# Kernel tuning notes

Measured on AMD Instinct MI355X. Metric: run time of the kernel, lower is better.

The kernel has to match this reference:

```python
import jax, jax.numpy as jnp
import numpy as np

S, B, E = 4096, 8, 1024
H, D, K = 16, 64, 64  # num_heads, head_dim, proj_dim
TAU = 1.0

def setup_inputs() -> dict:
    key = jax.random.key(0)
    ks = jax.random.split(key, 6)
    return {
        "encoder_output": jax.random.normal(ks[0], (S, B, E), dtype=jnp.float32),
        "Wk": jax.random.normal(ks[1], (E, E), dtype=jnp.float32) * (E ** -0.5),
        "bk": jax.random.normal(ks[2], (E,), dtype=jnp.float32) * 0.02,
        "Wv": jax.random.normal(ks[3], (E, E), dtype=jnp.float32) * (E ** -0.5),
        "bv": jax.random.normal(ks[4], (E,), dtype=jnp.float32) * 0.02,
        "random_matrices": jax.random.normal(ks[5], (H, K, D), dtype=jnp.float32),
        "mask": jnp.zeros((S, B, 1, 1), dtype=bool),
    }

def reference(encoder_output, Wk, bk, Wv, bv, random_matrices, mask):
    # k/v projections: [S,B,E] -> [S,B,H,D]
    k = (encoder_output @ Wk.T + bk).reshape(S, B, H, D)
    v = (encoder_output @ Wv.T + bv).reshape(S, B, H, D)
    # build_random_matrices (reparam_proj=False): divide by tau
    rm = random_matrices / TAU
    # rrf random feature map: scale by head_dim**-0.5 / tau, project, sin/cos concat
    x = k * (D ** -0.5) / TAU
    proj = jnp.einsum('sbhd,hkd->sbhk', x, rm)  # [S,B,H,K]
    phi_k = jnp.concatenate([jnp.sin(proj), jnp.cos(proj)], axis=-1) * (K ** -0.5)  # [S,B,H,2K]
    phi_k = jnp.where(mask, 0.0, phi_k)
    # s/z linear-attention state accumulation over seq_len
    s = jnp.einsum('sbhk,sbhd->bhkd', phi_k, v)  # [B,H,2K,D]
    z = jnp.sum(phi_k, axis=0)                   # [B,H,2K]
    return (s, z, rm)
```

## Files before the change

kernel.cpp:

```cpp
#include <hip/hip_runtime.h>
#include <hip/hip_bf16.h>
#include <stdint.h>


typedef short bf16x8 __attribute__((ext_vector_type(8)));
typedef float f32x4 __attribute__((ext_vector_type(4)));

__device__ __forceinline__ unsigned short f2bf(float f) {
  unsigned u = __float_as_uint(f);
  u += 0x7fffu + ((u >> 16) & 1u);
  return (unsigned short)(u >> 16);
}
__device__ __forceinline__ unsigned pack2(float a, float b) {
  return (unsigned)f2bf(a) | ((unsigned)f2bf(b) << 16);
}

#define OFF_WC   0ull
#define OFF_BC   4194304ull
#define OFF_AB   4202496ull
#define OFF_PS   272637952ull
#define OFF_PZ   306192384ull

__global__ __launch_bounds__(256) void k_conv_enc(const float* __restrict__ enc,
                                                  unsigned short* __restrict__ ab) {
  size_t i = ((size_t)blockIdx.x * 256 + threadIdx.x) * 8;
  const float4* p = (const float4*)(enc + i);
  float4 a = p[0], b = p[1];
  uint4 o;
  o.x = pack2(a.x, a.y); o.y = pack2(a.z, a.w);
  o.z = pack2(b.x, b.y); o.w = pack2(b.z, b.w);
  *(uint4*)(ab + i) = o;
}

__global__ __launch_bounds__(256) void k_prep_w(const float* __restrict__ Wk,
                                                const float* __restrict__ bk,
                                                const float* __restrict__ Wv,
                                                const float* __restrict__ bv,
                                                const float* __restrict__ rm,
                                                unsigned short* __restrict__ Wc,
                                                float* __restrict__ bc) {
  __shared__ float rv[64];
  int f = blockIdx.x;
  int tid = threadIdx.x;
  int e0 = tid * 4;
  if (f < 1024) {
    int h = f >> 6, kk = f & 63;
    if (tid < 64) rv[tid] = rm[(size_t)((h << 6) + kk) * 64 + tid] * 0.125f;
    __syncthreads();
    float a0 = 0.f, a1 = 0.f, a2 = 0.f, a3 = 0.f;
    const float* wbase = Wk + (size_t)(h << 6) * 1024 + e0;
    #pragma unroll 4
    for (int d = 0; d < 64; ++d) {
      float r = rv[d];
      const float4 w = *(const float4*)(wbase + (size_t)d * 1024);
      a0 += r * w.x; a1 += r * w.y; a2 += r * w.z; a3 += r * w.w;
    }
    uint2 o; o.x = pack2(a0, a1); o.y = pack2(a2, a3);
    *(uint2*)(Wc + (size_t)f * 1024 + e0) = o;
    if (tid == 0) {
      float s = 0.f;
      for (int d = 0; d < 64; ++d) s += rv[d] * bk[(h << 6) + d];
      bc[f] = s;
    }
  } else {
    int j = f - 1024;
    const float4 w = *(const float4*)(Wv + (size_t)j * 1024 + e0);
    uint2 o; o.x = pack2(w.x, w.y); o.y = pack2(w.z, w.w);
    *(uint2*)(Wc + (size_t)f * 1024 + e0) = o;
    if (tid == 0) bc[f] = bv[j];
  }
}

__global__ __launch_bounds__(256) void k_rm(const float* __restrict__ rm,
                                            float* __restrict__ out) {
  size_t i = ((size_t)blockIdx.x * 256 + threadIdx.x) * 4;
  *(float4*)(out + 1064960 + i) = *(const float4*)(rm + i);
}

__device__ __forceinline__ void glds16(const unsigned short* g, unsigned short* l) {
  __builtin_amdgcn_global_load_lds((const __attribute__((address_space(1))) unsigned int*)g,
                                   (__attribute__((address_space(3))) unsigned int*)l,
                                   16, 0, 0);
}

__global__ __launch_bounds__(256, 3) void k_fused(const unsigned short* __restrict__ Ab,
                                                  const unsigned short* __restrict__ Wc,
                                                  const float* __restrict__ bc,
                                                  float* __restrict__ ps,
                                                  float* __restrict__ pz) {
  __shared__ char smem[50176];
  unsigned short* As = (unsigned short*)smem;
  unsigned short* Bs = As + 128 * 64;
  unsigned short* Ph = (unsigned short*)smem;
  unsigned short* Vl = (unsigned short*)(smem + 32768);
  float* zbuf = (float*)(smem + 49152);

  const int bx = blockIdx.x;
  const int xcd = bx & 7;
  const int idx = bx >> 3;
  const int h = idx & 15;
  const int bcg = (idx >> 4) * 8 + xcd;
  const int b = bcg >> 3;
  const int sp = bcg & 7;
  const size_t bh = (size_t)b * 16 + h;

  const int tid = threadIdx.x;
  const int wave = tid >> 6;
  const int lane = tid & 63;
  const int wm = wave >> 1, wn = wave & 1;
  const int quad = lane >> 4, lm = lane & 15;
  const int lr = lane >> 3;
  const int lc = (((lane & 7) ^ lr) * 8);

  float biasj[4];
  int nrow[4];
  #pragma unroll
  for (int j = 0; j < 4; ++j) {
    if (j < 2) {
      nrow[j] = wn * 32 + j * 16 + lm;
      biasj[j] = bc[h * 64 + nrow[j]];
    } else {
      nrow[j] = 64 + wn * 32 + (j - 2) * 16 + lm;
      biasj[j] = bc[1024 + h * 64 + (nrow[j] - 64)];
    }
  }

  f32x4 acc2[2][4] = {};
  float zs[2] = {0.f, 0.f}, zc[2] = {0.f, 0.f};

  for (int st = 0; st < 4; ++st) {
    const int s_base = sp * 512 + st * 128;
    f32x4 acc[4][4] = {};

    for (int kt = 0; kt < 16; ++kt) {
      const int k0 = kt * 64;
      __syncthreads();
      #pragma unroll
      for (int c = 0; c < 4; ++c) {
        const int r = wave * 32 + c * 8;
        glds16(Ab + ((size_t)(s_base + r + lr) * 8 + b) * 1024 + k0 + lc, &As[r * 64]);
        const int rr = r + lr;
        const int wrow = h * 64 + rr + ((rr >= 64) ? 960 : 0);
        glds16(Wc + (size_t)wrow * 1024 + k0 + lc, &Bs[r * 64]);
      }
      __syncthreads();
      #pragma unroll
      for (int ks = 0; ks < 2; ++ks) {
        bf16x8 af[4], bfr[4];
        const int sw = ((ks * 4 + quad) ^ (lm & 7)) * 8;
        #pragma unroll
        for (int i = 0; i < 4; ++i)
          af[i] = *(const bf16x8*)&As[(wm * 64 + i * 16 + lm) * 64 + sw];
        #pragma unroll
        for (int j = 0; j < 4; ++j)
          bfr[j] = *(const bf16x8*)&Bs[nrow[j] * 64 + sw];
        #pragma unroll
        for (int i = 0; i < 4; ++i)
          #pragma unroll
          for (int j = 0; j < 4; ++j)
            acc[i][j] = __builtin_amdgcn_mfma_f32_16x16x32_bf16(af[i], bfr[j], acc[i][j], 0, 0, 0);
      }
    }

    __syncthreads();
    #pragma unroll
    for (int j = 0; j < 4; ++j) {
      #pragma unroll
      for (int i = 0; i < 4; ++i) {
        const int ch = wm * 8 + i * 2 + (quad >> 1);
        const int half = (quad & 1) * 4;
        if (j < 2) {
          const int kk = wn * 32 + j * 16 + lm;
          float sv[4], cv[4];
          #pragma unroll
          for (int r = 0; r < 4; ++r) {
            float p = acc[i][j][r] + biasj[j];
            __sincosf(p, &sv[r], &cv[r]);
            sv[r] *= 0.125f; cv[r] *= 0.125f;
          }
          zs[j] += sv[0] + sv[1] + sv[2] + sv[3];
          zc[j] += cv[0] + cv[1] + cv[2] + cv[3];
          uint2 os; os.x = pack2(sv[0], sv[1]); os.y = pack2(sv[2], sv[3]);
          uint2 oc; oc.x = pack2(cv[0], cv[1]); oc.y = pack2(cv[2], cv[3]);
          const int chs = (ch ^ (kk & 7)) * 8;
          *(uint2*)&Ph[kk * 128 + chs + half] = os;
          *(uint2*)&Ph[(kk + 64) * 128 + chs + half] = oc;
        } else {
          const int d = wn * 32 + (j - 2) * 16 + lm;
          uint2 ov;
          ov.x = pack2(acc[i][j][0] + biasj[j], acc[i][j][1] + biasj[j]);
          ov.y = pack2(acc[i][j][2] + biasj[j], acc[i][j][3] + biasj[j]);
          *(uint2*)&Vl[d * 128 + ((ch ^ (d & 7)) * 8) + half] = ov;
        }
      }
    }
    __syncthreads();

    #pragma unroll
    for (int ks2 = 0; ks2 < 4; ++ks2) {
      bf16x8 pa[2], vb[4];
      #pragma unroll
      for (int i2 = 0; i2 < 2; ++i2) {
        const int c = wave * 32 + i2 * 16 + lm;
        pa[i2] = *(const bf16x8*)&Ph[c * 128 + (((ks2 * 4 + quad) ^ (c & 7)) * 8)];
      }
      #pragma unroll
      for (int j2 = 0; j2 < 4; ++j2) {
        const int d = j2 * 16 + lm;
        vb[j2] = *(const bf16x8*)&Vl[d * 128 + (((ks2 * 4 + quad) ^ (d & 7)) * 8)];
      }
      #pragma unroll
      for (int i2 = 0; i2 < 2; ++i2)
        #pragma unroll
        for (int j2 = 0; j2 < 4; ++j2)
          acc2[i2][j2] = __builtin_amdgcn_mfma_f32_16x16x32_bf16(pa[i2], vb[j2], acc2[i2][j2], 0, 0, 0);
    }
  }

  float* po = ps + (size_t)sp * 1048576 + bh * 8192;
  #pragma unroll
  for (int i2 = 0; i2 < 2; ++i2) {
    #pragma unroll
    for (int j2 = 0; j2 < 4; ++j2) {
      const int d = j2 * 16 + lm;
      #pragma unroll
      for (int r = 0; r < 4; ++r) {
        const int c = wave * 32 + i2 * 16 + quad * 4 + r;
        po[(size_t)c * 64 + d] = acc2[i2][j2][r];
      }
    }
  }

  #pragma unroll
  for (int j = 0; j < 2; ++j) {
    zs[j] += __shfl_xor(zs[j], 16); zs[j] += __shfl_xor(zs[j], 32);
    zc[j] += __shfl_xor(zc[j], 16); zc[j] += __shfl_xor(zc[j], 32);
  }
  if (quad == 0) {
    #pragma unroll
    for (int j = 0; j < 2; ++j) {
      zbuf[wm * 128 + wn * 32 + j * 16 + lm] = zs[j];
      zbuf[wm * 128 + 64 + wn * 32 + j * 16 + lm] = zc[j];
    }
  }
  __syncthreads();
  if (tid < 128)
    pz[(size_t)sp * 16384 + bh * 128 + tid] = zbuf[tid] + zbuf[128 + tid];
}

__global__ __launch_bounds__(256) void k_reduce(const float* __restrict__ ps,
                                                const float* __restrict__ pz,
                                                float* __restrict__ out) {
  size_t i = ((size_t)blockIdx.x * 256 + threadIdx.x) * 4;
  if (i < 1048576) {
    float4 a = {0.f, 0.f, 0.f, 0.f};
    #pragma unroll
    for (int sp = 0; sp < 8; ++sp) {
      float4 x = *(const float4*)(ps + (size_t)sp * 1048576 + i);
      a.x += x.x; a.y += x.y; a.z += x.z; a.w += x.w;
    }
    *(float4*)(out + i) = a;
  } else if (i < 1064960) {
    size_t j = i - 1048576;
    float4 a = {0.f, 0.f, 0.f, 0.f};
    #pragma unroll
    for (int sp = 0; sp < 8; ++sp) {
      float4 x = *(const float4*)(pz + (size_t)sp * 16384 + j);
      a.x += x.x; a.y += x.y; a.z += x.z; a.w += x.w;
    }
    *(float4*)(out + 1048576 + j) = a;
  }
}

extern "C" void kernel_launch(void* const* d_in, const int* in_sizes, int n_in,
                              void* d_out, int out_size, void* d_ws, size_t ws_size,
                              hipStream_t stream) {
  (void)in_sizes; (void)n_in; (void)out_size; (void)ws_size;
  const float* enc = (const float*)d_in[0];
  const float* Wk  = (const float*)d_in[1];
  const float* bk  = (const float*)d_in[2];
  const float* Wv  = (const float*)d_in[3];
  const float* bv  = (const float*)d_in[4];
  const float* rm  = (const float*)d_in[5];
  float* out = (float*)d_out;
  char* ws = (char*)d_ws;
  unsigned short* Wc  = (unsigned short*)(ws + OFF_WC);
  float*          bc  = (float*)(ws + OFF_BC);
  unsigned short* Ab  = (unsigned short*)(ws + OFF_AB);
  float*          psp = (float*)(ws + OFF_PS);
  float*          pzp = (float*)(ws + OFF_PZ);

  hipLaunchKernelGGL(k_conv_enc, dim3(16384), dim3(256), 0, stream, enc, Ab);
  hipLaunchKernelGGL(k_prep_w,   dim3(2048),  dim3(256), 0, stream, Wk, bk, Wv, bv, rm, Wc, bc);
  hipLaunchKernelGGL(k_rm,       dim3(64),    dim3(256), 0, stream, rm, out);
  hipLaunchKernelGGL(k_fused,    dim3(1024),  dim3(256), 0, stream, Ab, Wc, bc, psp, pzp);
  hipLaunchKernelGGL(k_reduce,   dim3(1040),  dim3(256), 0, stream, psp, pzp, out);
}
```

Measured before the change: 438.3 us.

## Split sequence into 16 chunks, batch-major bf16 input, merged prep kernel

The three prep kernels (encoder bf16 conversion, weight fusion, rm copy) become one launch. The bf16 encoder copy is now stored batch-major, so each tile's rows are contiguous in memory. The fused GEMM/feature/state kernel doubles the sequence split from 8 to 16, giving 2048 blocks instead of 1024, which should improve wave balance across CUs. Partial s tiles are staged in LDS so they can be written with coalesced float4 stores. The cost is twice the partial-sum workspace traffic and a 16-way reduction.

```diff
diff --git a/kernel.cpp b/kernel.cpp
--- a/kernel.cpp
+++ b/kernel.cpp
@@ -18,63 +18,65 @@
 #define OFF_WC   0ull
 #define OFF_BC   4194304ull
 #define OFF_AB   4202496ull
-#define OFF_PS   272637952ull
-#define OFF_PZ   306192384ull
-
-__global__ __launch_bounds__(256) void k_conv_enc(const float* __restrict__ enc,
-                                                  unsigned short* __restrict__ ab) {
-  size_t i = ((size_t)blockIdx.x * 256 + threadIdx.x) * 8;
-  const float4* p = (const float4*)(enc + i);
-  float4 a = p[0], b = p[1];
-  uint4 o;
-  o.x = pack2(a.x, a.y); o.y = pack2(a.z, a.w);
-  o.z = pack2(b.x, b.y); o.w = pack2(b.z, b.w);
-  *(uint4*)(ab + i) = o;
-}
-
-__global__ __launch_bounds__(256) void k_prep_w(const float* __restrict__ Wk,
-                                                const float* __restrict__ bk,
-                                                const float* __restrict__ Wv,
-                                                const float* __restrict__ bv,
-                                                const float* __restrict__ rm,
-                                                unsigned short* __restrict__ Wc,
-                                                float* __restrict__ bc) {
-  __shared__ float rv[64];
-  int f = blockIdx.x;
-  int tid = threadIdx.x;
-  int e0 = tid * 4;
-  if (f < 1024) {
-    int h = f >> 6, kk = f & 63;
-    if (tid < 64) rv[tid] = rm[(size_t)((h << 6) + kk) * 64 + tid] * 0.125f;
-    __syncthreads();
-    float a0 = 0.f, a1 = 0.f, a2 = 0.f, a3 = 0.f;
-    const float* wbase = Wk + (size_t)(h << 6) * 1024 + e0;
-    #pragma unroll 4
-    for (int d = 0; d < 64; ++d) {
-      float r = rv[d];
-      const float4 w = *(const float4*)(wbase + (size_t)d * 1024);
-      a0 += r * w.x; a1 += r * w.y; a2 += r * w.z; a3 += r * w.w;
-    }
-    uint2 o; o.x = pack2(a0, a1); o.y = pack2(a2, a3);
-    *(uint2*)(Wc + (size_t)f * 1024 + e0) = o;
-    if (tid == 0) {
-      float s = 0.f;
-      for (int d = 0; d < 64; ++d) s += rv[d] * bk[(h << 6) + d];
-      bc[f] = s;
+#define OFF_PS   71311360ull
+#define OFF_PZ   138420224ull
+
+__global__ __launch_bounds__(256) void k_pre(const float* __restrict__ enc,
+                                             const float* __restrict__ Wk,
+                                             const float* __restrict__ bk,
+                                             const float* __restrict__ Wv,
+                                             const float* __restrict__ bv,
+                                             const float* __restrict__ rm,
+                                             unsigned short* __restrict__ ab,
+                                             unsigned short* __restrict__ Wc,
+                                             float* __restrict__ bc,
+                                             float* __restrict__ out) {
+  const int bid = blockIdx.x;
+  const int tid = threadIdx.x;
+  if (bid < 16384) {
+    const int r = bid * 2 + (tid >> 7);
+    const int e = (tid & 127) * 8;
+    const int s = r >> 3, b = r & 7;
+    const float4* p = (const float4*)(enc + (size_t)r * 1024 + e);
+    float4 a = p[0], b4 = p[1];
+    uint4 o;
+    o.x = pack2(a.x, a.y);  o.y = pack2(a.z, a.w);
+    o.z = pack2(b4.x, b4.y); o.w = pack2(b4.z, b4.w);
+    *(uint4*)(ab + ((size_t)b * 4096 + s) * 1024 + e) = o;
+  } else if (bid < 16384 + 2048) {
+    __shared__ float rv[64];
+    const int f = bid - 16384;
+    const int e0 = tid * 4;
+    if (f < 1024) {
+      int h = f >> 6, kk = f & 63;
+      if (tid < 64) rv[tid] = rm[(size_t)((h << 6) + kk) * 64 + tid] * 0.125f;
+      __syncthreads();
+      float a0 = 0.f, a1 = 0.f, a2 = 0.f, a3 = 0.f;
+      const float* wbase = Wk + (size_t)(h << 6) * 1024 + e0;
+      #pragma unroll 4
+      for (int d = 0; d < 64; ++d) {
+        float r = rv[d];
+        const float4 w = *(const float4*)(wbase + (size_t)d * 1024);
+        a0 += r * w.x; a1 += r * w.y; a2 += r * w.z; a3 += r * w.w;
+      }
+      uint2 o; o.x = pack2(a0, a1); o.y = pack2(a2, a3);
+      *(uint2*)(Wc + (size_t)f * 1024 + e0) = o;
+      if (tid == 0) {
+        float s = 0.f;
+        for (int d = 0; d < 64; ++d) s += rv[d] * bk[(h << 6) + d];
+        bc[f] = s;
+      }
+    } else {
+      int j = f - 1024;
+      const float4 w = *(const float4*)(Wv + (size_t)j * 1024 + e0);
+      uint2 o; o.x = pack2(w.x, w.y); o.y = pack2(w.z, w.w);
+      *(uint2*)(Wc + (size_t)f * 1024 + e0) = o;
+      if (tid == 0) bc[f] = bv[j];
     }
   } else {
-    int j = f - 1024;
-    const float4 w = *(const float4*)(Wv + (size_t)j * 1024 + e0);
-    uint2 o; o.x = pack2(w.x, w.y); o.y = pack2(w.z, w.w);
-    *(uint2*)(Wc + (size_t)f * 1024 + e0) = o;
-    if (tid == 0) bc[f] = bv[j];
-  }
-}
-
-__global__ __launch_bounds__(256) void k_rm(const float* __restrict__ rm,
-                                            float* __restrict__ out) {
-  size_t i = ((size_t)blockIdx.x * 256 + threadIdx.x) * 4;
-  *(float4*)(out + 1064960 + i) = *(const float4*)(rm + i);
+    size_t i = ((size_t)(bid - 18432) * 256 + tid) * 4;
+    *(float4*)(out + 1064960 + i) = *(const float4*)(rm + i);
+  }
 }
 
 __device__ __forceinline__ void glds16(const unsigned short* g, unsigned short* l) {
@@ -94,14 +96,15 @@
   unsigned short* Ph = (unsigned short*)smem;
   unsigned short* Vl = (unsigned short*)(smem + 32768);
   float* zbuf = (float*)(smem + 49152);
+  float* Psf  = (float*)smem;
 
   const int bx = blockIdx.x;
   const int xcd = bx & 7;
   const int idx = bx >> 3;
   const int h = idx & 15;
   const int bcg = (idx >> 4) * 8 + xcd;
-  const int b = bcg >> 3;
-  const int sp = bcg & 7;
+  const int b = bcg >> 4;
+  const int sp = bcg & 15;
   const size_t bh = (size_t)b * 16 + h;
 
   const int tid = threadIdx.x;
@@ -128,8 +131,8 @@
   f32x4 acc2[2][4] = {};
   float zs[2] = {0.f, 0.f}, zc[2] = {0.f, 0.f};
 
-  for (int st = 0; st < 4; ++st) {
-    const int s_base = sp * 512 + st * 128;
+  for (int st = 0; st < 2; ++st) {
+    const int s_base = sp * 256 + st * 128;
     f32x4 acc[4][4] = {};
 
     for (int kt = 0; kt < 16; ++kt) {
@@ -138,7 +141,7 @@
       #pragma unroll
       for (int c = 0; c < 4; ++c) {
         const int r = wave * 32 + c * 8;
-        glds16(Ab + ((size_t)(s_base + r + lr) * 8 + b) * 1024 + k0 + lc, &As[r * 64]);
+        glds16(Ab + ((size_t)b * 4096 + s_base + r + lr) * 1024 + k0 + lc, &As[r * 64]);
         const int rr = r + lr;
         const int wrow = h * 64 + rr + ((rr >= 64) ? 960 : 0);
         glds16(Wc + (size_t)wrow * 1024 + k0 + lc, &Bs[r * 64]);
@@ -217,19 +220,18 @@
     }
   }
 
-  float* po = ps + (size_t)sp * 1048576 + bh * 8192;
+  __syncthreads();
   #pragma unroll
-  for (int i2 = 0; i2 < 2; ++i2) {
+  for (int i2 = 0; i2 < 2; ++i2)
     #pragma unroll
     for (int j2 = 0; j2 < 4; ++j2) {
       const int d = j2 * 16 + lm;
       #pragma unroll
       for (int r = 0; r < 4; ++r) {
         const int c = wave * 32 + i2 * 16 + quad * 4 + r;
-        po[(size_t)c * 64 + d] = acc2[i2][j2][r];
-      }
-    }
-  }
+        Psf[c * 64 + d] = acc2[i2][j2][r];
+      }
+    }
 
   #pragma unroll
   for (int j = 0; j < 2; ++j) {
@@ -244,6 +246,13 @@
     }
   }
   __syncthreads();
+
+  float* po = ps + (size_t)sp * 1048576 + bh * 8192;
+  #pragma unroll
+  for (int rr = 0; rr < 8; ++rr) {
+    const int f = rr * 256 + tid;
+    ((float4*)po)[f] = ((const float4*)Psf)[f];
+  }
   if (tid < 128)
     pz[(size_t)sp * 16384 + bh * 128 + tid] = zbuf[tid] + zbuf[128 + tid];
 }
@@ -255,7 +264,7 @@
   if (i < 1048576) {
     float4 a = {0.f, 0.f, 0.f, 0.f};
     #pragma unroll
-    for (int sp = 0; sp < 8; ++sp) {
+    for (int sp = 0; sp < 16; ++sp) {
       float4 x = *(const float4*)(ps + (size_t)sp * 1048576 + i);
       a.x += x.x; a.y += x.y; a.z += x.z; a.w += x.w;
     }
@@ -264,7 +273,7 @@
     size_t j = i - 1048576;
     float4 a = {0.f, 0.f, 0.f, 0.f};
     #pragma unroll
-    for (int sp = 0; sp < 8; ++sp) {
+    for (int sp = 0; sp < 16; ++sp) {
       float4 x = *(const float4*)(pz + (size_t)sp * 16384 + j);
       a.x += x.x; a.y += x.y; a.z += x.z; a.w += x.w;
     }
@@ -290,9 +299,8 @@
   float*          psp = (float*)(ws + OFF_PS);
   float*          pzp = (float*)(ws + OFF_PZ);
 
-  hipLaunchKernelGGL(k_conv_enc, dim3(16384), dim3(256), 0, stream, enc, Ab);
-  hipLaunchKernelGGL(k_prep_w,   dim3(2048),  dim3(256), 0, stream, Wk, bk, Wv, bv, rm, Wc, bc);
-  hipLaunchKernelGGL(k_rm,       dim3(64),    dim3(256), 0, stream, rm, out);
-  hipLaunchKernelGGL(k_fused,    dim3(1024),  dim3(256), 0, stream, Ab, Wc, bc, psp, pzp);
-  hipLaunchKernelGGL(k_reduce,   dim3(1040),  dim3(256), 0, stream, psp, pzp, out);
-}
+  hipLaunchKernelGGL(k_pre,    dim3(18496), dim3(256), 0, stream,
+                     enc, Wk, bk, Wv, bv, rm, Ab, Wc, bc, out);
+  hipLaunchKernelGGL(k_fused,  dim3(2048),  dim3(256), 0, stream, Ab, Wc, bc, psp, pzp);
+  hipLaunchKernelGGL(k_reduce, dim3(1040),  dim3(256), 0, stream, psp, pzp, out);
+}
```

Measured after the change: 406.3 us. -7.3%, faster.
